# Kernel optimization log

Measured on AMD Instinct MI355X. Metric: run time of the kernel, lower is better.

The kernel has to match this reference:

```python
import jax, jax.numpy as jnp
import numpy as np

B, N, H = 32, 1024, 256
ALPHA = 0.2  # leaky relu slope
NEG_INF = -1e12


def setup_inputs() -> dict:
    key = jax.random.key(0)
    k1, k2, k3, k4, k5, k6 = jax.random.split(key, 6)
    inp = jax.random.normal(k1, (B, N, H), dtype=jnp.float32)
    A = (jax.random.uniform(k2, (B, N, N)) < 0.05).astype(jnp.float32)
    l = jnp.sort(jax.random.randint(k3, (B, 2), 0, N), axis=1)
    # xavier-uniform(gain=1.414) approximated; exact init values are irrelevant for correctness
    lim_w = 1.414 * np.sqrt(6.0 / (H + H))
    W_i = jax.random.uniform(k4, (H, H), minval=-lim_w, maxval=lim_w, dtype=jnp.float32)
    W_c = jax.random.uniform(k5, (H, H), minval=-lim_w, maxval=lim_w, dtype=jnp.float32)
    lim_a = 1.414 * np.sqrt(6.0 / (2 * H + 1))
    a = jax.random.uniform(k6, (2 * H, 1), minval=-lim_a, maxval=lim_a, dtype=jnp.float32)
    return {"inp": inp, "A": A, "l": l, "W_i": W_i, "W_c": W_c, "a": a}


def reference(inp, A, l, W_i, W_c, a):
    # eval mode: dropout is identity (training=False)
    n = inp.shape[1]
    h = inp.shape[2]
    Wh_i = jnp.einsum('bnh,he->bne', inp, W_i)
    Wh_c = jnp.einsum('bnh,he->bne', inp, W_c)
    # vectorized replacement of the per-batch Wh[index][i:j] = Wh_i[index][i:j] loop
    idx = jnp.arange(n)
    sel = (idx[None, :] >= l[:, 0:1]) & (idx[None, :] < l[:, 1:2])  # [B,N]
    Wh = jnp.where(sel[:, :, None], Wh_i, Wh_c)
    # additive attention scores
    Wh1 = Wh @ a[:h, :]  # [B,N,1]
    Wh2 = Wh @ a[h:, :]  # [B,N,1]
    A_ = A + jnp.eye(n, dtype=A.dtype)
    e = jax.nn.leaky_relu((Wh1 + jnp.swapaxes(Wh2, 1, 2)) * A_, ALPHA)
    att = jnp.where(A_ > 0, e, NEG_INF)
    att = jax.nn.softmax(att, axis=2)
    h_prime = jnp.einsum('bnm,bme->bne', att, Wh)
    return jax.nn.elu(h_prime)  # concat=True
```

## Files before the change

kernel.cpp:

```cpp
#include <hip/hip_runtime.h>
#include <hip/hip_bf16.h>
#include <stdint.h>

#define B_ 32
#define N_ 1024
#define H_ 256

typedef short bf16x8 __attribute__((ext_vector_type(8)));
typedef float floatx4 __attribute__((ext_vector_type(4)));

__device__ inline unsigned short f2bs(float x) {
    __hip_bfloat16 h = __float2bfloat16(x);
    return __builtin_bit_cast(unsigned short, h);
}

__global__ __launch_bounds__(256)
void k_uvec(const float* __restrict__ Wi, const float* __restrict__ Wc,
            const float* __restrict__ a, float* __restrict__ U) {
    int k = blockIdx.x;
    int t = threadIdx.x;
    float wi = Wi[k * H_ + t];
    float wc = Wc[k * H_ + t];
    float a1 = a[t], a2 = a[H_ + t];
    float p0 = wi * a1, p1 = wc * a1, p2 = wi * a2, p3 = wc * a2;
    for (int off = 32; off; off >>= 1) {
        p0 += __shfl_xor(p0, off);
        p1 += __shfl_xor(p1, off);
        p2 += __shfl_xor(p2, off);
        p3 += __shfl_xor(p3, off);
    }
    __shared__ float red[4][4];
    int w = t >> 6;
    if ((t & 63) == 0) { red[w][0] = p0; red[w][1] = p1; red[w][2] = p2; red[w][3] = p3; }
    __syncthreads();
    if (t == 0) {
        U[0 * H_ + k] = red[0][0] + red[1][0] + red[2][0] + red[3][0];
        U[1 * H_ + k] = red[0][1] + red[1][1] + red[2][1] + red[3][1];
        U[2 * H_ + k] = red[0][2] + red[1][2] + red[2][2] + red[3][2];
        U[3 * H_ + k] = red[0][3] + red[1][3] + red[2][3] + red[3][3];
    }
}

__global__ __launch_bounds__(256)
void k_prep(const float* __restrict__ Wi, const float* __restrict__ Wc,
            unsigned short* __restrict__ WtFi, unsigned short* __restrict__ WtFc) {
    __shared__ float tile[64][65];
    int mat = blockIdx.x >> 4;
    int tr = ((blockIdx.x >> 2) & 3) * 64;
    int tc = (blockIdx.x & 3) * 64;
    const float* W = mat ? Wc : Wi;
    unsigned short* WtF = mat ? WtFc : WtFi;
    int t = threadIdx.x;
    int rr = t >> 2, c4 = (t & 3) * 16;
    const float* src = W + (size_t)(tr + rr) * H_ + tc + c4;
#pragma unroll
    for (int j = 0; j < 4; ++j) {
        float4 v = *reinterpret_cast<const float4*>(src + j * 4);
        tile[rr][c4 + 4 * j + 0] = v.x;
        tile[rr][c4 + 4 * j + 1] = v.y;
        tile[rr][c4 + 4 * j + 2] = v.z;
        tile[rr][c4 + 4 * j + 3] = v.w;
    }
    __syncthreads();
#pragma unroll
    for (int h = 0; h < 2; ++h) {
        int s = h * 256 + t;
        int ksl = s >> 8;
        int cl  = (s >> 6) & 3;
        int ll  = s & 63;
        int m16v = ll & 15, quadv = ll >> 4;
        int nloc = cl * 16 + m16v;
        int kb = ksl * 32 + quadv * 8;
        unsigned int pk[4];
#pragma unroll
        for (int jj = 0; jj < 4; ++jj) {
            unsigned short lo = f2bs(tile[kb + 2 * jj][nloc]);
            unsigned short hi = f2bs(tile[kb + 2 * jj + 1][nloc]);
            pk[jj] = (unsigned int)lo | ((unsigned int)hi << 16);
        }
        int ksg = (tr >> 5) + ksl;
        int cg  = (tc >> 4) + cl;
        *reinterpret_cast<uint4*>(WtF + ((size_t)(ksg * 16 + cg) * 64 + ll) * 8) =
            *reinterpret_cast<uint4*>(pk);
    }
}

__global__ __launch_bounds__(256)
void k_wh12(const float* __restrict__ inp, const int* __restrict__ l,
            const float* __restrict__ U,
            float* __restrict__ Wh1, float* __restrict__ Wh2,
            unsigned short* __restrict__ inpb) {
    int w = threadIdx.x >> 6, lane = threadIdx.x & 63;
    int row = blockIdx.x * 4 + w;
    int b = row >> 10, n = row & (N_ - 1);
    int l0 = l[2 * b], l1 = l[2 * b + 1];
    bool sel = (n >= l0) && (n < l1);
    const float* u1 = U + (sel ? 0 : H_);
    const float* u2 = U + 2 * H_ + (sel ? 0 : H_);
    const float4 x  = *reinterpret_cast<const float4*>(inp + (size_t)row * H_ + lane * 4);
    const float4 c1 = *reinterpret_cast<const float4*>(u1 + lane * 4);
    const float4 c2 = *reinterpret_cast<const float4*>(u2 + lane * 4);
    unsigned int p0 = (unsigned int)f2bs(x.x) | ((unsigned int)f2bs(x.y) << 16);
    unsigned int p1 = (unsigned int)f2bs(x.z) | ((unsigned int)f2bs(x.w) << 16);
    uint2 pk = {p0, p1};
    *reinterpret_cast<uint2*>(inpb + (size_t)row * H_ + lane * 4) = pk;

    float d1 = x.x * c1.x + x.y * c1.y + x.z * c1.z + x.w * c1.w;
    float d2 = x.x * c2.x + x.y * c2.y + x.z * c2.z + x.w * c2.w;
    for (int off = 32; off; off >>= 1) {
        d1 += __shfl_xor(d1, off);
        d2 += __shfl_xor(d2, off);
    }
    if (lane == 0) { Wh1[row] = d1; Wh2[row] = d2; }
}

__global__ __launch_bounds__(256)
void k_gemm(const unsigned short* __restrict__ inpb, const int* __restrict__ l,
            const unsigned short* __restrict__ WtFi, const unsigned short* __restrict__ WtFc,
            __hip_bfloat16* __restrict__ Whb) {
    __shared__ unsigned short bbuf[2][4096];
    int blk = blockIdx.x;
    int b  = blk >> 5;
    int r0 = ((blk >> 1) & 15) * 64;
    int n0 = (blk & 1) * 128;
    int t = threadIdx.x;
    int lane = t & 63;
    int quad = lane >> 4, m16 = lane & 15;
    int rowb = r0 + (t >> 6) * 16;

    int l0 = l[2 * b], l1 = l[2 * b + 1];
    bool allI = (l0 <= r0) && (r0 + 64 <= l1);
    bool allC = (l1 <= r0) || (l0 >= r0 + 64);
    int npass = (allI || allC) ? 1 : 2;

    const unsigned short* arow = inpb + ((size_t)(b * N_ + rowb + m16)) * H_ + quad * 8;
    __hip_bfloat16* obase = Whb + ((size_t)(b * N_ + rowb)) * H_ + n0;
    int cb = n0 >> 4;

    for (int pass = 0; pass < npass; ++pass) {
        const unsigned short* WtF =
            (npass == 1) ? (allI ? WtFi : WtFc) : (pass == 0 ? WtFi : WtFc);
        const unsigned short* gbase = WtF + cb * 512;

        floatx4 acc[8];
#pragma unroll
        for (int c = 0; c < 8; ++c) acc[c] = (floatx4){0.f, 0.f, 0.f, 0.f};

        {
            uint4 v0 = *reinterpret_cast<const uint4*>(gbase + (size_t)t * 8);
            uint4 v1 = *reinterpret_cast<const uint4*>(gbase + (size_t)(256 + t) * 8);
            *reinterpret_cast<uint4*>(&bbuf[0][t * 8]) = v0;
            *reinterpret_cast<uint4*>(&bbuf[0][(256 + t) * 8]) = v1;
        }
        for (int ks = 0; ks < 8; ++ks) {
            __syncthreads();
            uint4 v0, v1;
            if (ks < 7) {
                v0 = *reinterpret_cast<const uint4*>(gbase + (size_t)(ks + 1) * 8192 + t * 8);
                v1 = *reinterpret_cast<const uint4*>(gbase + (size_t)(ks + 1) * 8192 + (256 + t) * 8);
            }
            bf16x8 af = *reinterpret_cast<const bf16x8*>(arow + ks * 32);
            const unsigned short* bptr = &bbuf[ks & 1][lane * 8];
#pragma unroll
            for (int c = 0; c < 8; ++c) {
                bf16x8 bfr = *reinterpret_cast<const bf16x8*>(bptr + c * 512);
                acc[c] = __builtin_amdgcn_mfma_f32_16x16x32_bf16(af, bfr, acc[c], 0, 0, 0);
            }
            if (ks < 7) {
                *reinterpret_cast<uint4*>(&bbuf[(ks + 1) & 1][t * 8]) = v0;
                *reinterpret_cast<uint4*>(&bbuf[(ks + 1) & 1][(256 + t) * 8]) = v1;
            }
        }
        __syncthreads();

#pragma unroll
        for (int c = 0; c < 8; ++c) {
#pragma unroll
            for (int r = 0; r < 4; ++r) {
                int n = rowb + quad * 4 + r;
                bool sel = (n >= l0) && (n < l1);
                bool doit = (npass == 1) || (pass == 0 ? sel : !sel);
                if (doit)
                    obase[(size_t)(quad * 4 + r) * H_ + c * 16 + m16] =
                        __float2bfloat16(acc[c][r]);
            }
        }
    }
}

__global__ __launch_bounds__(256)
void k_attn(const float* __restrict__ A, const float* __restrict__ Wh1,
            const float* __restrict__ Wh2, const __hip_bfloat16* __restrict__ Whb,
            float* __restrict__ out) {
    __shared__ float sc[N_];
    __shared__ float ps[N_];
    __shared__ unsigned short idxs[N_];
    __shared__ float red[8];
    __shared__ int cnt;

    int t = threadIdx.x;
    int w = t >> 6, lane = t & 63;
    int row = blockIdx.x;
    int b = row >> 10, i = row & (N_ - 1);
    if (t == 0) cnt = 0;

    float wh1 = Wh1[row];
    const float* Arow = A + (size_t)row * N_;
    const float* Wh2b = Wh2 + b * N_;
    const float NEGINF = -__builtin_inff();

    int idx4 = t * 4;
    float4 av = *reinterpret_cast<const float4*>(Arow + idx4);
    if ((i >> 2) == t) ((float*)&av)[i & 3] += 1.0f;
    float4 w2 = *reinterpret_cast<const float4*>(Wh2b + idx4);
    float lmax = -1e30f;
    {
        const float aa[4] = {av.x, av.y, av.z, av.w};
        const float ww[4] = {w2.x, w2.y, w2.z, w2.w};
        float e[4];
#pragma unroll
        for (int c = 0; c < 4; ++c) {
            float p  = (wh1 + ww[c]) * aa[c];
            float lv = p >= 0.f ? p : 0.2f * p;
            e[c] = aa[c] > 0.f ? lv : NEGINF;
            lmax = fmaxf(lmax, e[c]);
        }
        float4 ev; ev.x = e[0]; ev.y = e[1]; ev.z = e[2]; ev.w = e[3];
        *reinterpret_cast<float4*>(sc + idx4) = ev;
    }
    for (int off = 32; off; off >>= 1) lmax = fmaxf(lmax, __shfl_xor(lmax, off));
    if (lane == 0) red[w] = lmax;
    __syncthreads();
    float bmax = fmaxf(fmaxf(red[0], red[1]), fmaxf(red[2], red[3]));

    float lsum = 0.f;
#pragma unroll
    for (int q = 0; q < 4; ++q) {
        int j = (w * 4 + q) * 64 + lane;
        float ev = sc[j];
        bool nz = ev > -1e30f;
        float p = nz ? __expf(ev - bmax) : 0.f;
        lsum += p;
        unsigned long long mask = __ballot(nz);
        int base = 0;
        if (lane == 0) base = atomicAdd(&cnt, __popcll(mask));
        base = __shfl(base, 0);
        if (nz) {
            int pos = base + __popcll(mask & ((1ull << lane) - 1ull));
            ps[pos] = p;
            idxs[pos] = (unsigned short)j;
        }
    }
    for (int off = 32; off; off >>= 1) lsum += __shfl_xor(lsum, off);
    if (lane == 0) red[4 + w] = lsum;
    __syncthreads();
    float scale = 1.0f / (red[4] + red[5] + red[6] + red[7]);
    int T = cnt;

    float4 acc = {0.f, 0.f, 0.f, 0.f};
    const __hip_bfloat16* Whbase = Whb + (size_t)b * N_ * H_;
    int tb = (T * w) >> 2;
    int te = (T * (w + 1)) >> 2;
    int tt = tb;
    for (; tt + 8 <= te; tt += 8) {
        int jj[8]; float pv[8];
#pragma unroll
        for (int u = 0; u < 8; ++u) { jj[u] = idxs[tt + u]; pv[u] = ps[tt + u]; }
        uint2 d[8];
#pragma unroll
        for (int u = 0; u < 8; ++u)
            d[u] = *reinterpret_cast<const uint2*>(Whbase + (size_t)jj[u] * H_ + lane * 4);
#pragma unroll
        for (int u = 0; u < 8; ++u) {
            acc.x += pv[u] * __uint_as_float(d[u].x << 16);
            acc.y += pv[u] * __uint_as_float(d[u].x & 0xffff0000u);
            acc.z += pv[u] * __uint_as_float(d[u].y << 16);
            acc.w += pv[u] * __uint_as_float(d[u].y & 0xffff0000u);
        }
    }
    for (; tt < te; ++tt) {
        int jj = idxs[tt]; float pv = ps[tt];
        uint2 d = *reinterpret_cast<const uint2*>(Whbase + (size_t)jj * H_ + lane * 4);
        acc.x += pv * __uint_as_float(d.x << 16);
        acc.y += pv * __uint_as_float(d.x & 0xffff0000u);
        acc.z += pv * __uint_as_float(d.y << 16);
        acc.w += pv * __uint_as_float(d.y & 0xffff0000u);
    }

    *reinterpret_cast<float4*>(sc + w * 256 + lane * 4) = acc;
    __syncthreads();
    float o = sc[t] + sc[256 + t] + sc[512 + t] + sc[768 + t];
    o *= scale;
    o = o > 0.f ? o : __expf(o) - 1.0f;
    out[(size_t)row * H_ + t] = o;
}

extern "C" void kernel_launch(void* const* d_in, const int* in_sizes, int n_in,
                              void* d_out, int out_size, void* d_ws, size_t ws_size,
                              hipStream_t stream) {
    const float* inp = (const float*)d_in[0];
    const float* A   = (const float*)d_in[1];
    const int*   l   = (const int*)d_in[2];
    const float* Wi  = (const float*)d_in[3];
    const float* Wc  = (const float*)d_in[4];
    const float* a   = (const float*)d_in[5];
    float* out = (float*)d_out;

    char* ws = (char*)d_ws;
    size_t off = 0;
    __hip_bfloat16* Whb = (__hip_bfloat16*)(ws + off); off += (size_t)B_ * N_ * H_ * 2;
    unsigned short* inpb = (unsigned short*)(ws + off); off += (size_t)B_ * N_ * H_ * 2;
    float* Wh1 = (float*)(ws + off); off += (size_t)B_ * N_ * 4;
    float* Wh2 = (float*)(ws + off); off += (size_t)B_ * N_ * 4;
    float* U   = (float*)(ws + off); off += 4 * H_ * 4;
    unsigned short* WtFi = (unsigned short*)(ws + off); off += (size_t)H_ * H_ * 2;
    unsigned short* WtFc = (unsigned short*)(ws + off); off += (size_t)H_ * H_ * 2;

    k_uvec<<<H_, 256, 0, stream>>>(Wi, Wc, a, U);
    k_prep<<<32, 256, 0, stream>>>(Wi, Wc, WtFi, WtFc);
    k_wh12<<<(B_ * N_) / 4, 256, 0, stream>>>(inp, l, U, Wh1, Wh2, inpb);
    k_gemm<<<B_ * 16 * 2, 256, 0, stream>>>(inpb, l, WtFi, WtFc, Whb);
    k_attn<<<B_ * N_, 256, 0, stream>>>(A, Wh1, Wh2, Whb, out);
}
```

Baseline: 330.8 us.

## Compute attention aggregation as dense bf16 MFMA over 16-row tiles

```diff
diff --git a/kernel.cpp b/kernel.cpp
--- a/kernel.cpp
+++ b/kernel.cpp
@@ -117,16 +117,17 @@
 __global__ __launch_bounds__(256)
 void k_gemm(const unsigned short* __restrict__ inpb, const int* __restrict__ l,
             const unsigned short* __restrict__ WtFi, const unsigned short* __restrict__ WtFc,
-            __hip_bfloat16* __restrict__ Whb) {
+            unsigned short* __restrict__ WhF) {
     __shared__ unsigned short bbuf[2][4096];
     int blk = blockIdx.x;
     int b  = blk >> 5;
     int r0 = ((blk >> 1) & 15) * 64;
     int n0 = (blk & 1) * 128;
     int t = threadIdx.x;
+    int w = t >> 6;
     int lane = t & 63;
     int quad = lane >> 4, m16 = lane & 15;
-    int rowb = r0 + (t >> 6) * 16;
+    int rowb = r0 + w * 16;
 
     int l0 = l[2 * b], l1 = l[2 * b + 1];
     bool allI = (l0 <= r0) && (r0 + 64 <= l1);
@@ -134,8 +135,13 @@
     int npass = (allI || allC) ? 1 : 2;
 
     const unsigned short* arow = inpb + ((size_t)(b * N_ + rowb + m16)) * H_ + quad * 8;
-    __hip_bfloat16* obase = Whb + ((size_t)(b * N_ + rowb)) * H_ + n0;
+    unsigned short* fb = WhF + (size_t)b * (N_ * H_);
     int cb = n0 >> 4;
+
+    int j0 = rowb + quad * 4;
+    int ksO = j0 >> 5;
+    int laneF = m16 + 16 * ((j0 & 31) >> 3);
+    int jj0 = j0 & 7;
 
     for (int pass = 0; pass < npass; ++pass) {
         const unsigned short* WtF =
@@ -175,14 +181,31 @@
 
 #pragma unroll
         for (int c = 0; c < 8; ++c) {
-#pragma unroll
-            for (int r = 0; r < 4; ++r) {
-                int n = rowb + quad * 4 + r;
-                bool sel = (n >= l0) && (n < l1);
-                bool doit = (npass == 1) || (pass == 0 ? sel : !sel);
-                if (doit)
-                    obase[(size_t)(quad * 4 + r) * H_ + c * 16 + m16] =
-                        __float2bfloat16(acc[c][r]);
+            size_t base = ((size_t)((ksO * 16 + cb + c) * 64) + laneF) * 8 + jj0;
+            if (npass == 1) {
+                unsigned int lo = (unsigned int)f2bs(acc[c][0]) | ((unsigned int)f2bs(acc[c][1]) << 16);
+                unsigned int hi = (unsigned int)f2bs(acc[c][2]) | ((unsigned int)f2bs(acc[c][3]) << 16);
+                uint2 v = {lo, hi};
+                *reinterpret_cast<uint2*>(fb + base) = v;
+            } else {
+                bool want[4]; bool all = true, none = true;
+#pragma unroll
+                for (int r = 0; r < 4; ++r) {
+                    int j = j0 + r;
+                    bool sel = (j >= l0) && (j < l1);
+                    want[r] = (pass == 0) ? sel : !sel;
+                    all = all && want[r]; none = none && !want[r];
+                }
+                if (all) {
+                    unsigned int lo = (unsigned int)f2bs(acc[c][0]) | ((unsigned int)f2bs(acc[c][1]) << 16);
+                    unsigned int hi = (unsigned int)f2bs(acc[c][2]) | ((unsigned int)f2bs(acc[c][3]) << 16);
+                    uint2 v = {lo, hi};
+                    *reinterpret_cast<uint2*>(fb + base) = v;
+                } else if (!none) {
+#pragma unroll
+                    for (int r = 0; r < 4; ++r)
+                        if (want[r]) fb[base + r] = f2bs(acc[c][r]);
+                }
             }
         }
     }
@@ -190,109 +213,99 @@
 
 __global__ __launch_bounds__(256)
 void k_attn(const float* __restrict__ A, const float* __restrict__ Wh1,
-            const float* __restrict__ Wh2, const __hip_bfloat16* __restrict__ Whb,
+            const float* __restrict__ Wh2, const unsigned short* __restrict__ WhF,
             float* __restrict__ out) {
-    __shared__ float sc[N_];
-    __shared__ float ps[N_];
-    __shared__ unsigned short idxs[N_];
-    __shared__ float red[8];
-    __shared__ int cnt;
-
-    int t = threadIdx.x;
-    int w = t >> 6, lane = t & 63;
-    int row = blockIdx.x;
-    int b = row >> 10, i = row & (N_ - 1);
-    if (t == 0) cnt = 0;
-
-    float wh1 = Wh1[row];
-    const float* Arow = A + (size_t)row * N_;
+    __shared__ unsigned short pfrag[32 * 520];
+    __shared__ float scl[16];
+    int t = threadIdx.x, w = t >> 6, lane = t & 63;
+    int bi = blockIdx.x;
+    int b = (bi & 7) + 8 * (bi >> 9);
+    int tile = (bi >> 3) & 63;
+    int rowbase = tile * 16;
+
     const float* Wh2b = Wh2 + b * N_;
-    const float NEGINF = -__builtin_inff();
-
-    int idx4 = t * 4;
-    float4 av = *reinterpret_cast<const float4*>(Arow + idx4);
-    if ((i >> 2) == t) ((float*)&av)[i & 3] += 1.0f;
-    float4 w2 = *reinterpret_cast<const float4*>(Wh2b + idx4);
-    float lmax = -1e30f;
-    {
-        const float aa[4] = {av.x, av.y, av.z, av.w};
-        const float ww[4] = {w2.x, w2.y, w2.z, w2.w};
-        float e[4];
-#pragma unroll
-        for (int c = 0; c < 4; ++c) {
-            float p  = (wh1 + ww[c]) * aa[c];
-            float lv = p >= 0.f ? p : 0.2f * p;
-            e[c] = aa[c] > 0.f ? lv : NEGINF;
-            lmax = fmaxf(lmax, e[c]);
-        }
-        float4 ev; ev.x = e[0]; ev.y = e[1]; ev.z = e[2]; ev.w = e[3];
-        *reinterpret_cast<float4*>(sc + idx4) = ev;
-    }
-    for (int off = 32; off; off >>= 1) lmax = fmaxf(lmax, __shfl_xor(lmax, off));
-    if (lane == 0) red[w] = lmax;
+    float4 w2v[4];
+#pragma unroll
+    for (int ch = 0; ch < 4; ++ch)
+        w2v[ch] = *reinterpret_cast<const float4*>(Wh2b + ch * 256 + lane * 4);
+
+    int ksl = lane >> 3;
+    int q2 = (lane >> 1) & 3;
+    int jj0 = (lane & 1) * 4;
+
+#pragma unroll
+    for (int q = 0; q < 4; ++q) {
+        int m = w * 4 + q;
+        int i = rowbase + m;
+        float wh1 = Wh1[b * N_ + i];
+        const float* Arow = A + ((size_t)(b * N_ + i)) * N_;
+        float e[16];
+        float lmax = -1e30f;
+#pragma unroll
+        for (int ch = 0; ch < 4; ++ch) {
+            float4 av = *reinterpret_cast<const float4*>(Arow + ch * 256 + lane * 4);
+            if ((i >> 2) == (ch * 64 + lane)) ((float*)&av)[i & 3] += 1.0f;
+            float aa[4] = {av.x, av.y, av.z, av.w};
+            float ww[4] = {w2v[ch].x, w2v[ch].y, w2v[ch].z, w2v[ch].w};
+#pragma unroll
+            for (int c = 0; c < 4; ++c) {
+                float p = (wh1 + ww[c]) * aa[c];
+                float lv = fmaxf(p, 0.2f * p);
+                e[ch * 4 + c] = aa[c] > 0.f ? lv : -1e30f;
+                lmax = fmaxf(lmax, e[ch * 4 + c]);
+            }
+        }
+        for (int off = 32; off; off >>= 1) lmax = fmaxf(lmax, __shfl_xor(lmax, off));
+
+        float lsum = 0.f;
+        unsigned int pk[8];
+#pragma unroll
+        for (int h2 = 0; h2 < 8; ++h2) {
+            float p0 = e[2 * h2]     > -1e29f ? __expf(e[2 * h2]     - lmax) : 0.f;
+            float p1 = e[2 * h2 + 1] > -1e29f ? __expf(e[2 * h2 + 1] - lmax) : 0.f;
+            lsum += p0 + p1;
+            pk[h2] = (unsigned int)f2bs(p0) | ((unsigned int)f2bs(p1) << 16);
+        }
+        for (int off = 32; off; off >>= 1) lsum += __shfl_xor(lsum, off);
+        if (lane == 0) scl[m] = 1.0f / lsum;
+
+#pragma unroll
+        for (int ch = 0; ch < 4; ++ch) {
+            int ks = ch * 8 + ksl;
+            uint2 v = {pk[2 * ch], pk[2 * ch + 1]};
+            *reinterpret_cast<uint2*>(pfrag + ks * 520 + (m + 16 * q2) * 8 + jj0) = v;
+        }
+    }
     __syncthreads();
-    float bmax = fmaxf(fmaxf(red[0], red[1]), fmaxf(red[2], red[3]));
-
-    float lsum = 0.f;
-#pragma unroll
-    for (int q = 0; q < 4; ++q) {
-        int j = (w * 4 + q) * 64 + lane;
-        float ev = sc[j];
-        bool nz = ev > -1e30f;
-        float p = nz ? __expf(ev - bmax) : 0.f;
-        lsum += p;
-        unsigned long long mask = __ballot(nz);
-        int base = 0;
-        if (lane == 0) base = atomicAdd(&cnt, __popcll(mask));
-        base = __shfl(base, 0);
-        if (nz) {
-            int pos = base + __popcll(mask & ((1ull << lane) - 1ull));
-            ps[pos] = p;
-            idxs[pos] = (unsigned short)j;
-        }
-    }
-    for (int off = 32; off; off >>= 1) lsum += __shfl_xor(lsum, off);
-    if (lane == 0) red[4 + w] = lsum;
-    __syncthreads();
-    float scale = 1.0f / (red[4] + red[5] + red[6] + red[7]);
-    int T = cnt;
-
-    float4 acc = {0.f, 0.f, 0.f, 0.f};
-    const __hip_bfloat16* Whbase = Whb + (size_t)b * N_ * H_;
-    int tb = (T * w) >> 2;
-    int te = (T * (w + 1)) >> 2;
-    int tt = tb;
-    for (; tt + 8 <= te; tt += 8) {
-        int jj[8]; float pv[8];
-#pragma unroll
-        for (int u = 0; u < 8; ++u) { jj[u] = idxs[tt + u]; pv[u] = ps[tt + u]; }
-        uint2 d[8];
-#pragma unroll
-        for (int u = 0; u < 8; ++u)
-            d[u] = *reinterpret_cast<const uint2*>(Whbase + (size_t)jj[u] * H_ + lane * 4);
-#pragma unroll
-        for (int u = 0; u < 8; ++u) {
-            acc.x += pv[u] * __uint_as_float(d[u].x << 16);
-            acc.y += pv[u] * __uint_as_float(d[u].x & 0xffff0000u);
-            acc.z += pv[u] * __uint_as_float(d[u].y << 16);
-            acc.w += pv[u] * __uint_as_float(d[u].y & 0xffff0000u);
-        }
-    }
-    for (; tt < te; ++tt) {
-        int jj = idxs[tt]; float pv = ps[tt];
-        uint2 d = *reinterpret_cast<const uint2*>(Whbase + (size_t)jj * H_ + lane * 4);
-        acc.x += pv * __uint_as_float(d.x << 16);
-        acc.y += pv * __uint_as_float(d.x & 0xffff0000u);
-        acc.z += pv * __uint_as_float(d.y << 16);
-        acc.w += pv * __uint_as_float(d.y & 0xffff0000u);
-    }
-
-    *reinterpret_cast<float4*>(sc + w * 256 + lane * 4) = acc;
-    __syncthreads();
-    float o = sc[t] + sc[256 + t] + sc[512 + t] + sc[768 + t];
-    o *= scale;
-    o = o > 0.f ? o : __expf(o) - 1.0f;
-    out[(size_t)row * H_ + t] = o;
+
+    const unsigned short* WB = WhF + (size_t)b * (N_ * H_);
+    floatx4 acc[4];
+#pragma unroll
+    for (int cc = 0; cc < 4; ++cc) acc[cc] = (floatx4){0.f, 0.f, 0.f, 0.f};
+#pragma unroll 2
+    for (int ks = 0; ks < 32; ++ks) {
+        bf16x8 af = *reinterpret_cast<const bf16x8*>(pfrag + ks * 520 + lane * 8);
+#pragma unroll
+        for (int cc = 0; cc < 4; ++cc) {
+            int c = w * 4 + cc;
+            bf16x8 bfv = *reinterpret_cast<const bf16x8*>(
+                WB + ((size_t)((ks * 16 + c) * 64 + lane)) * 8);
+            acc[cc] = __builtin_amdgcn_mfma_f32_16x16x32_bf16(af, bfv, acc[cc], 0, 0, 0);
+        }
+    }
+
+    int quad = lane >> 4, m16 = lane & 15;
+#pragma unroll
+    for (int cc = 0; cc < 4; ++cc) {
+        int col = (w * 4 + cc) * 16 + m16;
+#pragma unroll
+        for (int r = 0; r < 4; ++r) {
+            int m = quad * 4 + r;
+            float v = acc[cc][r] * scl[m];
+            v = v > 0.f ? v : __expf(v) - 1.0f;
+            out[((size_t)(b * N_ + rowbase + m)) * H_ + col] = v;
+        }
+    }
 }
 
 extern "C" void kernel_launch(void* const* d_in, const int* in_sizes, int n_in,
@@ -308,7 +321,7 @@
 
     char* ws = (char*)d_ws;
     size_t off = 0;
-    __hip_bfloat16* Whb = (__hip_bfloat16*)(ws + off); off += (size_t)B_ * N_ * H_ * 2;
+    unsigned short* WhF  = (unsigned short*)(ws + off); off += (size_t)B_ * N_ * H_ * 2;
     unsigned short* inpb = (unsigned short*)(ws + off); off += (size_t)B_ * N_ * H_ * 2;
     float* Wh1 = (float*)(ws + off); off += (size_t)B_ * N_ * 4;
     float* Wh2 = (float*)(ws + off); off += (size_t)B_ * N_ * 4;
@@ -319,6 +332,6 @@
     k_uvec<<<H_, 256, 0, stream>>>(Wi, Wc, a, U);
     k_prep<<<32, 256, 0, stream>>>(Wi, Wc, WtFi, WtFc);
     k_wh12<<<(B_ * N_) / 4, 256, 0, stream>>>(inp, l, U, Wh1, Wh2, inpb);
-    k_gemm<<<B_ * 16 * 2, 256, 0, stream>>>(inpb, l, WtFi, WtFc, Whb);
-    k_attn<<<B_ * N_, 256, 0, stream>>>(A, Wh1, Wh2, Whb, out);
-}
+    k_gemm<<<B_ * 16 * 2, 256, 0, stream>>>(inpb, l, WtFi, WtFc, WhF);
+    k_attn<<<B_ * (N_ / 16), 256, 0, stream>>>(A, Wh1, Wh2, WhF, out);
+}
```

After: 294.4 us. 1.12x faster.
